# Kernel tuning notes

Hardware: AMD Instinct MI355X
Metric: run time of the kernel (lower is better)

The kernel has to match this reference:

```python
import jax, jax.numpy as jnp
import numpy as np

N = 100000      # num nodes
E = 1600000     # num edges
IN = 128        # in_channels
OUT = 128       # out_channels
K = 2           # num_k_hops


def setup_inputs() -> dict:
    key = jax.random.key(0)
    k1, k2, k3 = jax.random.split(key, 3)
    x = jax.random.normal(k1, (N, IN), dtype=jnp.float32)
    edge_index = jax.random.randint(k2, (2, E), 0, N, dtype=jnp.int32)
    # Linear(in, out) params, kaiming-uniform-ish scale
    W = jax.random.normal(k3, (OUT, IN), dtype=jnp.float32) * (1.0 / np.sqrt(IN))
    b = jnp.zeros((OUT,), dtype=jnp.float32)
    return {"x": x, "edge_index": edge_index, "W": W, "b": b}


def reference(x, edge_index, W, b):
    n = x.shape[0]
    # gcn_norm: add self-loops, symmetric normalization deg^-1/2 A_hat deg^-1/2
    loop = jnp.arange(n, dtype=edge_index.dtype)
    row = jnp.concatenate([edge_index[0], loop])  # source j
    col = jnp.concatenate([edge_index[1], loop])  # target i
    deg = jax.ops.segment_sum(jnp.ones_like(col, dtype=x.dtype), col, num_segments=n)
    dinv = jnp.where(deg > 0, jax.lax.rsqrt(deg), jnp.zeros_like(deg))
    norm = dinv[row] * dinv[col]  # [E+N]

    def hop(h, _):
        # out[i] = sum_{(j->i)} norm_ij * h[j]  (gather + scatter-add SpMM)
        msg = norm[:, None] * h[row]
        return jax.ops.segment_sum(msg, col, num_segments=n), None

    h, _ = jax.lax.scan(hop, x, None, length=K)
    # final linear projection (SGConv.lin)
    return h @ W.T + b
```

## Files before the change

kernel.cpp:

```cpp
#include <hip/hip_runtime.h>

#define CAP 64
#define NPB 256
#define NPB_SHIFT 8
#define CAPB 4864
#define EPB 8192
#define MAXB 512

typedef __attribute__((ext_vector_type(8))) short short8v;
typedef __attribute__((ext_vector_type(4))) float f32x4;

__device__ __forceinline__ unsigned f2bf(float f) {
  unsigned u = __float_as_uint(f);
  u += 0x7fffu + ((u >> 16) & 1u);
  return u >> 16;
}
__device__ __forceinline__ float bflo(unsigned u) { return __uint_as_float(u << 16); }
__device__ __forceinline__ float bfhi(unsigned u) { return __uint_as_float(u & 0xffff0000u); }

__global__ __launch_bounds__(256) void k_binA(const int* __restrict__ row,
                                              const int* __restrict__ col,
                                              int* __restrict__ gcur,
                                              unsigned int* __restrict__ binned,
                                              int E, int nb) {
  __shared__ int lcnt[MAXB];
  int tid = threadIdx.x;
  for (int i = tid; i < nb; i += 256) lcnt[i] = 0;
  __syncthreads();
  int e0 = blockIdx.x * EPB;
#pragma unroll
  for (int it = 0; it < EPB / 256; ++it) {
    int e = e0 + it * 256 + tid;
    if (e < E) atomicAdd(&lcnt[col[e] >> NPB_SHIFT], 1);
  }
  __syncthreads();
  for (int b = tid; b < nb; b += 256) {
    int c = lcnt[b];
    lcnt[b] = (c > 0) ? atomicAdd(&gcur[b], c) : 0;
  }
  __syncthreads();
#pragma unroll
  for (int it = 0; it < EPB / 256; ++it) {
    int e = e0 + it * 256 + tid;
    if (e < E) {
      int c = col[e];
      int s = row[e];
      int b = c >> NPB_SHIFT;
      int pos = atomicAdd(&lcnt[b], 1);
      if (pos < (b + 1) * CAPB)
        binned[pos] = ((unsigned)s << NPB_SHIFT) | (unsigned)(c & (NPB - 1));
    }
  }
}

__global__ __launch_bounds__(256) void k_binB(const unsigned int* __restrict__ binned,
                                              const int* __restrict__ gcur,
                                              int* __restrict__ counts,
                                              float* __restrict__ dinv,
                                              int* __restrict__ srcbuf,
                                              int N) {
  __shared__ int cur[NPB];
  int tid = threadIdx.x;
  int b = blockIdx.x;
  cur[tid] = 0;
  __syncthreads();
  int cnt = gcur[b] - b * CAPB;
  if (cnt > CAPB) cnt = CAPB;
  const unsigned int* bp = binned + (size_t)b * CAPB;
  int nb0 = b << NPB_SHIFT;
  for (int e = tid; e < cnt; e += 256) {
    unsigned p = bp[e];
    int li = p & (NPB - 1);
    int s = (int)(p >> NPB_SHIFT);
    int r = atomicAdd(&cur[li], 1);
    if (r < CAP - 1) srcbuf[((size_t)(nb0 + li) << 6) + r] = s;
  }
  __syncthreads();
  int node = nb0 + tid;
  if (node < N) {
    int c = cur[tid];
    int mlen = (c < CAP - 1) ? c : (CAP - 1);
    int* myp = srcbuf + ((size_t)node << 6);
    myp[mlen] = node;
    int cntp = (mlen + 1 + 7) & ~7;
    for (int p2 = mlen + 1; p2 < cntp; ++p2) myp[p2] = N;
    counts[node] = cntp;
    dinv[node] = rsqrtf((float)c + 1.0f);
  }
}

__global__ void k_init(int* __restrict__ gcur, int nb) {
  int i = blockIdx.x * blockDim.x + threadIdx.x;
  if (i < nb) gcur[i] = i * CAPB;
}

__global__ __launch_bounds__(256) void k_prescale(const float2* __restrict__ x2,
                                                  const float* __restrict__ dinv,
                                                  unsigned* __restrict__ xb,
                                                  int n64) {
  int i = blockIdx.x * blockDim.x + threadIdx.x;
  if (i >= n64) return;
  float d = dinv[i >> 6];
  float2 v = x2[i];
  xb[i] = f2bf(v.x * d) | (f2bf(v.y * d) << 16);
}

#define ACC8(v)                          \
  a[0] += bflo((v).x); a[1] += bfhi((v).x); \
  a[2] += bflo((v).y); a[3] += bfhi((v).y); \
  a[4] += bflo((v).z); a[5] += bfhi((v).z); \
  a[6] += bflo((v).w); a[7] += bfhi((v).w);

template <int MODE>
__global__ __launch_bounds__(256) void k_hop(
    const unsigned* __restrict__ hin, unsigned* __restrict__ hout,
    const int* __restrict__ srcbuf, const int* __restrict__ counts,
    const float* __restrict__ dinv, int n) {
  int wave = __builtin_amdgcn_readfirstlane((int)(threadIdx.x >> 6));
  int lane = threadIdx.x & 63;
  int node = blockIdx.x * 4 + wave;
  if (node >= n) return;
  int cntp = counts[node];
  float di = dinv[node];
  int g = lane >> 4;
  int m = lane & 15;
  const uint4* h4 = (const uint4*)hin;
  const int* sp = srcbuf + ((size_t)node << 6);
  float a[8];
#pragma unroll
  for (int i = 0; i < 8; ++i) a[i] = 0.f;
  int e = 0;
  for (; e + 16 <= cntp; e += 16) {
    int s0 = sp[e + g];
    int s1 = sp[e + 4 + g];
    int s2 = sp[e + 8 + g];
    int s3 = sp[e + 12 + g];
    uint4 v0 = h4[((size_t)s0 << 4) + m];
    uint4 v1 = h4[((size_t)s1 << 4) + m];
    uint4 v2 = h4[((size_t)s2 << 4) + m];
    uint4 v3 = h4[((size_t)s3 << 4) + m];
    ACC8(v0); ACC8(v1); ACC8(v2); ACC8(v3);
  }
  if (e < cntp) {
    int s0 = sp[e + g];
    int s1 = sp[e + 4 + g];
    uint4 v0 = h4[((size_t)s0 << 4) + m];
    uint4 v1 = h4[((size_t)s1 << 4) + m];
    ACC8(v0); ACC8(v1);
  }
#pragma unroll
  for (int i = 0; i < 8; ++i) {
    a[i] += __shfl_xor(a[i], 32);
    a[i] += __shfl_xor(a[i], 16);
  }
  float s = (MODE == 1) ? di * di : di;
  unsigned o = f2bf(a[2 * g] * s) | (f2bf(a[2 * g + 1] * s) << 16);
  hout[((size_t)node << 6) + (m << 2) + g] = o;
}

__global__ __launch_bounds__(256) void k_gemm_mfma(
    const unsigned* __restrict__ h2b, const float* __restrict__ W,
    const float* __restrict__ bias, float* __restrict__ out, int n) {
  __shared__ short Wl[128 * 128];
  int tid = threadIdx.x;
  const float4* Wg4 = (const float4*)W;
#pragma unroll
  for (int it = 0; it < 8; ++it) {
    int idx = tid + (it << 8);
    int c = idx >> 4;
    int j = idx & 15;
    float4 a = Wg4[c * 32 + j * 2];
    float4 bq = Wg4[c * 32 + j * 2 + 1];
    short8v s;
    s[0] = (short)f2bf(a.x);  s[1] = (short)f2bf(a.y);
    s[2] = (short)f2bf(a.z);  s[3] = (short)f2bf(a.w);
    s[4] = (short)f2bf(bq.x); s[5] = (short)f2bf(bq.y);
    s[6] = (short)f2bf(bq.z); s[7] = (short)f2bf(bq.w);
    int eo = (j << 3) ^ ((c & 7) << 3);
    *(short8v*)&Wl[(c << 7) + eo] = s;
  }
  __syncthreads();

  int wv = __builtin_amdgcn_readfirstlane((int)(tid >> 6));
  int lane = tid & 63;
  int tiles = (n + 15) >> 4;
  int tile = blockIdx.x * 4 + wv;
  if (tile >= tiles) return;
  int row0 = tile << 4;
  int r = lane & 15, g = lane >> 4;

  int arow = row0 + r;
  if (arow >= n) arow = n - 1;
  const short* hrow = (const short*)(h2b + ((size_t)arow << 6));
  short8v A0 = *(const short8v*)&hrow[g * 8];
  short8v A1 = *(const short8v*)&hrow[g * 8 + 32];
  short8v A2 = *(const short8v*)&hrow[g * 8 + 64];
  short8v A3 = *(const short8v*)&hrow[g * 8 + 96];

#pragma unroll
  for (int ct = 0; ct < 8; ++ct) {
    int c = (ct << 4) + r;
    int sw = (c & 7) << 3;
    const short* wrow = &Wl[c << 7];
    short8v B0 = *(const short8v*)&wrow[(g * 8) ^ sw];
    short8v B1 = *(const short8v*)&wrow[(g * 8 + 32) ^ sw];
    short8v B2 = *(const short8v*)&wrow[(g * 8 + 64) ^ sw];
    short8v B3 = *(const short8v*)&wrow[(g * 8 + 96) ^ sw];
    f32x4 acc = {0.f, 0.f, 0.f, 0.f};
    acc = __builtin_amdgcn_mfma_f32_16x16x32_bf16(A0, B0, acc, 0, 0, 0);
    acc = __builtin_amdgcn_mfma_f32_16x16x32_bf16(A1, B1, acc, 0, 0, 0);
    acc = __builtin_amdgcn_mfma_f32_16x16x32_bf16(A2, B2, acc, 0, 0, 0);
    acc = __builtin_amdgcn_mfma_f32_16x16x32_bf16(A3, B3, acc, 0, 0, 0);
    float bb = bias[c];
#pragma unroll
    for (int q = 0; q < 4; ++q) {
      int rr = row0 + g * 4 + q;
      if (rr < n) out[(size_t)rr * 128 + c] = acc[q] + bb;
    }
  }
}

extern "C" void kernel_launch(void* const* d_in, const int* in_sizes, int n_in,
                              void* d_out, int out_size, void* d_ws, size_t ws_size,
                              hipStream_t stream) {
  const float* x = (const float*)d_in[0];
  const int* ei = (const int*)d_in[1];
  const float* W = (const float*)d_in[2];
  const float* b = (const float*)d_in[3];
  int N = in_sizes[0] / 128;
  int E = in_sizes[1] / 2;
  float* out = (float*)d_out;

  char* ws = (char*)d_ws;
  int* counts = (int*)ws;
  float* dinv = (float*)(ws + (512u << 10));
  int* gcur = (int*)(ws + (960u << 10));
  int* srcbuf = (int*)(ws + (1u << 20));
  unsigned* xb = (unsigned*)(ws + (27u << 20));
  unsigned* h2b = xb;
  unsigned* h1b = (unsigned*)(ws + (53u << 20));
  unsigned int* binned = (unsigned int*)(ws + (53u << 20));

  int nb = (N + NPB - 1) >> NPB_SHIFT;
  int blocksA = (E + EPB - 1) / EPB;
  int tiles = (N + 15) >> 4;

  hipMemsetAsync(xb + ((size_t)N << 6), 0, 256, stream);
  hipMemsetAsync(h1b + ((size_t)N << 6), 0, 256, stream);

  k_init<<<(nb + 255) / 256, 256, 0, stream>>>(gcur, nb);
  k_binA<<<blocksA, 256, 0, stream>>>(ei, ei + E, gcur, binned, E, nb);
  k_binB<<<nb, 256, 0, stream>>>(binned, gcur, counts, dinv, srcbuf, N);
  k_prescale<<<(N * 64 + 255) / 256, 256, 0, stream>>>((const float2*)x, dinv, xb, N * 64);
  k_hop<1><<<(N + 3) / 4, 256, 0, stream>>>(xb, h1b, srcbuf, counts, dinv, N);
  k_hop<2><<<(N + 3) / 4, 256, 0, stream>>>(h1b, h2b, srcbuf, counts, dinv, N);
  k_gemm_mfma<<<(tiles + 3) / 4, 256, 0, stream>>>(h2b, W, b, out, N);
}
```

Baseline: 209.9 us.

## Process two nodes per wave in hop kernel with bpermute-broadcast neighbor indices

Each wavefront now aggregates two destination nodes at once, so twice as many independent gathers are in flight per loop iteration. The neighbor index list is loaded once per lane and distributed with ds_bpermute instead of repeated scalar-indexed loads. Out-of-range slots point at a zeroed padding row, which removes the tail branch, and results are written as full 16-byte stores from one lane group. The cost is that each pair iterates to the larger of the two degree counts and register pressure rises.

```diff
diff --git a/kernel.cpp b/kernel.cpp
--- a/kernel.cpp
+++ b/kernel.cpp
@@ -9,6 +9,7 @@
 
 typedef __attribute__((ext_vector_type(8))) short short8v;
 typedef __attribute__((ext_vector_type(4))) float f32x4;
+typedef __attribute__((ext_vector_type(2))) float f32x2;
 
 __device__ __forceinline__ unsigned f2bf(float f) {
   unsigned u = __float_as_uint(f);
@@ -105,11 +106,12 @@
   xb[i] = f2bf(v.x * d) | (f2bf(v.y * d) << 16);
 }
 
-#define ACC8(v)                          \
-  a[0] += bflo((v).x); a[1] += bfhi((v).x); \
-  a[2] += bflo((v).y); a[3] += bfhi((v).y); \
-  a[4] += bflo((v).z); a[5] += bfhi((v).z); \
-  a[6] += bflo((v).w); a[7] += bfhi((v).w);
+__device__ __forceinline__ void acc8(f32x2* A, uint4 v) {
+  A[0].x += bflo(v.x); A[0].y += bfhi(v.x);
+  A[1].x += bflo(v.y); A[1].y += bfhi(v.y);
+  A[2].x += bflo(v.z); A[2].y += bfhi(v.z);
+  A[3].x += bflo(v.w); A[3].y += bfhi(v.w);
+}
 
 template <int MODE>
 __global__ __launch_bounds__(256) void k_hop(
@@ -118,44 +120,75 @@
     const float* __restrict__ dinv, int n) {
   int wave = __builtin_amdgcn_readfirstlane((int)(threadIdx.x >> 6));
   int lane = threadIdx.x & 63;
-  int node = blockIdx.x * 4 + wave;
-  if (node >= n) return;
-  int cntp = counts[node];
-  float di = dinv[node];
+  int base = blockIdx.x * 8 + wave * 2;
+  if (base >= n) return;
+  int n0 = base;
+  int n1 = (base + 1 < n) ? base + 1 : base;
+  int c0 = counts[n0];
+  int c1 = counts[n1];
+  int cmax = (c0 > c1) ? c0 : c1;
+  int s0 = srcbuf[((size_t)n0 << 6) + lane];
+  int s1 = srcbuf[((size_t)n1 << 6) + lane];
+  s0 = (lane < c0) ? s0 : n;
+  s1 = (lane < c1) ? s1 : n;
+  float di0 = dinv[n0];
+  float di1 = dinv[n1];
   int g = lane >> 4;
   int m = lane & 15;
-  const uint4* h4 = (const uint4*)hin;
-  const int* sp = srcbuf + ((size_t)node << 6);
-  float a[8];
-#pragma unroll
-  for (int i = 0; i < 8; ++i) a[i] = 0.f;
-  int e = 0;
-  for (; e + 16 <= cntp; e += 16) {
-    int s0 = sp[e + g];
-    int s1 = sp[e + 4 + g];
-    int s2 = sp[e + 8 + g];
-    int s3 = sp[e + 12 + g];
-    uint4 v0 = h4[((size_t)s0 << 4) + m];
-    uint4 v1 = h4[((size_t)s1 << 4) + m];
-    uint4 v2 = h4[((size_t)s2 << 4) + m];
-    uint4 v3 = h4[((size_t)s3 << 4) + m];
-    ACC8(v0); ACC8(v1); ACC8(v2); ACC8(v3);
-  }
-  if (e < cntp) {
-    int s0 = sp[e + g];
-    int s1 = sp[e + 4 + g];
-    uint4 v0 = h4[((size_t)s0 << 4) + m];
-    uint4 v1 = h4[((size_t)s1 << 4) + m];
-    ACC8(v0); ACC8(v1);
-  }
-#pragma unroll
-  for (int i = 0; i < 8; ++i) {
-    a[i] += __shfl_xor(a[i], 32);
-    a[i] += __shfl_xor(a[i], 16);
-  }
-  float s = (MODE == 1) ? di * di : di;
-  unsigned o = f2bf(a[2 * g] * s) | (f2bf(a[2 * g + 1] * s) << 16);
-  hout[((size_t)node << 6) + (m << 2) + g] = o;
+  int g4 = g << 2;
+  const char* hb = (const char*)hin;
+  unsigned bm = (unsigned)(m << 4);
+  f32x2 A0[4], A1[4];
+#pragma unroll
+  for (int q = 0; q < 4; ++q) { A0[q] = (f32x2){0.f, 0.f}; A1[q] = (f32x2){0.f, 0.f}; }
+
+  for (int e = 0; e < cmax; e += 16) {
+    int i0 = __builtin_amdgcn_ds_bpermute(((e) << 2) + (g4 << 0), s0);
+    int i1 = __builtin_amdgcn_ds_bpermute(((e + 4) << 2) + g4, s0);
+    int i2 = __builtin_amdgcn_ds_bpermute(((e + 8) << 2) + g4, s0);
+    int i3 = __builtin_amdgcn_ds_bpermute(((e + 12) << 2) + g4, s0);
+    int j0 = __builtin_amdgcn_ds_bpermute(((e) << 2) + g4, s1);
+    int j1 = __builtin_amdgcn_ds_bpermute(((e + 4) << 2) + g4, s1);
+    int j2 = __builtin_amdgcn_ds_bpermute(((e + 8) << 2) + g4, s1);
+    int j3 = __builtin_amdgcn_ds_bpermute(((e + 12) << 2) + g4, s1);
+    uint4 v0 = *(const uint4*)(hb + (((size_t)(unsigned)i0 << 8) + bm));
+    uint4 v1 = *(const uint4*)(hb + (((size_t)(unsigned)i1 << 8) + bm));
+    uint4 v2 = *(const uint4*)(hb + (((size_t)(unsigned)i2 << 8) + bm));
+    uint4 v3 = *(const uint4*)(hb + (((size_t)(unsigned)i3 << 8) + bm));
+    uint4 w0 = *(const uint4*)(hb + (((size_t)(unsigned)j0 << 8) + bm));
+    uint4 w1 = *(const uint4*)(hb + (((size_t)(unsigned)j1 << 8) + bm));
+    uint4 w2 = *(const uint4*)(hb + (((size_t)(unsigned)j2 << 8) + bm));
+    uint4 w3 = *(const uint4*)(hb + (((size_t)(unsigned)j3 << 8) + bm));
+    acc8(A0, v0); acc8(A0, v1); acc8(A0, v2); acc8(A0, v3);
+    acc8(A1, w0); acc8(A1, w1); acc8(A1, w2); acc8(A1, w3);
+  }
+
+  float sc0 = (MODE == 1) ? di0 * di0 : di0;
+  float sc1 = (MODE == 1) ? di1 * di1 : di1;
+#pragma unroll
+  for (int q = 0; q < 4; ++q) {
+    float x = A0[q].x, y = A0[q].y;
+    x += __shfl_xor(x, 32); x += __shfl_xor(x, 16);
+    y += __shfl_xor(y, 32); y += __shfl_xor(y, 16);
+    A0[q].x = x * sc0; A0[q].y = y * sc0;
+    float u = A1[q].x, v = A1[q].y;
+    u += __shfl_xor(u, 32); u += __shfl_xor(u, 16);
+    v += __shfl_xor(v, 32); v += __shfl_xor(v, 16);
+    A1[q].x = u * sc1; A1[q].y = v * sc1;
+  }
+  if (g == 0) {
+    uint4 o0, o1;
+    o0.x = f2bf(A0[0].x) | (f2bf(A0[0].y) << 16);
+    o0.y = f2bf(A0[1].x) | (f2bf(A0[1].y) << 16);
+    o0.z = f2bf(A0[2].x) | (f2bf(A0[2].y) << 16);
+    o0.w = f2bf(A0[3].x) | (f2bf(A0[3].y) << 16);
+    o1.x = f2bf(A1[0].x) | (f2bf(A1[0].y) << 16);
+    o1.y = f2bf(A1[1].x) | (f2bf(A1[1].y) << 16);
+    o1.z = f2bf(A1[2].x) | (f2bf(A1[2].y) << 16);
+    o1.w = f2bf(A1[3].x) | (f2bf(A1[3].y) << 16);
+    *(uint4*)&hout[((size_t)n0 << 6) + (m << 2)] = o0;
+    *(uint4*)&hout[((size_t)n1 << 6) + (m << 2)] = o1;
+  }
 }
 
 __global__ __launch_bounds__(256) void k_gemm_mfma(
@@ -252,7 +285,7 @@
   k_binA<<<blocksA, 256, 0, stream>>>(ei, ei + E, gcur, binned, E, nb);
   k_binB<<<nb, 256, 0, stream>>>(binned, gcur, counts, dinv, srcbuf, N);
   k_prescale<<<(N * 64 + 255) / 256, 256, 0, stream>>>((const float2*)x, dinv, xb, N * 64);
-  k_hop<1><<<(N + 3) / 4, 256, 0, stream>>>(xb, h1b, srcbuf, counts, dinv, N);
-  k_hop<2><<<(N + 3) / 4, 256, 0, stream>>>(h1b, h2b, srcbuf, counts, dinv, N);
+  k_hop<1><<<(N + 7) / 8, 256, 0, stream>>>(xb, h1b, srcbuf, counts, dinv, N);
+  k_hop<2><<<(N + 7) / 8, 256, 0, stream>>>(h1b, h2b, srcbuf, counts, dinv, N);
   k_gemm_mfma<<<(tiles + 3) / 4, 256, 0, stream>>>(h2b, W, b, out, N);
 }
```

Result: slower. 215.3 us (+2.6%).
